# Optimization experiments

Measured on AMD Instinct MI355X. Metric: run time of the kernel, lower is better.

## Reference

```python
import jax
import jax.numpy as jnp
import numpy as np
from jax import lax


def setup_inputs() -> dict:
    key = jax.random.key(0)
    k0, k1 = jax.random.split(key)
    B, C, H, W = 8, 256, 96, 96
    FM0 = jax.random.normal(k0, (B, C, H, W), dtype=jnp.float32)
    FM1 = jax.random.normal(k1, (B, C, H, W), dtype=jnp.float32)
    return {"FM0": FM0, "FM1": FM1, "d_max": 4, "stride": 1}


def pointwise_correlation(FM0, FM1, d_max, stride):
    """out[b,h,w,i,j] = sum_c FM0[b,c,h,w] * FM1[b,c,h+(i-d)*s, w+(j-d)*s],
    with zero padding outside FM1's spatial extent."""
    B, C, H, W = FM0.shape
    D = 2 * d_max + 1
    p = d_max * stride
    FM1p = jnp.pad(FM1, ((0, 0), (0, 0), (p, p), (p, p)))
    offs = jnp.arange(D, dtype=jnp.int32) * stride  # start offsets into padded map
    ys, xs = jnp.meshgrid(offs, offs, indexing="ij")
    offsets = jnp.stack([ys.ravel(), xs.ravel()], axis=-1)  # (D*D, 2)

    def step(carry, off):
        sl = lax.dynamic_slice(FM1p, (0, 0, off[0], off[1]), (B, C, H, W))
        corr = jnp.einsum("bchw,bchw->bhw", FM0, sl)
        return carry, corr

    _, out = lax.scan(step, None, offsets)  # (D*D, B, H, W)
    out = out.reshape(D, D, B, H, W).transpose(2, 3, 4, 0, 1)  # (B, H, W, D, D)
    return out


def reference(FM0, FM1, d_max, stride):
    return pointwise_correlation(FM0, FM1, d_max, stride)
```

## Files before the change

kernel.cpp:

```cpp
#include <hip/hip_runtime.h>

#define HH 96
#define WW 96
#define CC 256
#define PLANE (HH * WW)
#define PITCH 40
#define AROWS 144
#define BROWS 704
#define LDSN ((AROWS + BROWS) * PITCH)
#define NOUT 81
#define NGRP 1696
#define GPT 5

typedef __attribute__((ext_vector_type(4))) float f32x4;
typedef __attribute__((ext_vector_type(2))) unsigned int u32x2;
typedef __attribute__((ext_vector_type(8))) __bf16 bf16x8;

static __device__ __forceinline__ unsigned int pkbf(float x, float y) {
  unsigned int ux = __builtin_bit_cast(unsigned int, x) + 0x8000u;
  unsigned int uy = __builtin_bit_cast(unsigned int, y) + 0x8000u;
  return __builtin_amdgcn_perm(uy, ux, 0x07060302u);
}

#define BAR_LGKM() asm volatile("s_waitcnt lgkmcnt(0)\n\ts_barrier" ::: "memory")

__global__ __launch_bounds__(384, 2) void corr_kernel(
    const float* __restrict__ fm0, const float* __restrict__ fm1,
    float* __restrict__ out) {
  __shared__ __align__(16) unsigned short lds[2 * LDSN];

  const int tid = threadIdx.x;
  const int bid = blockIdx.x;
  const int b = bid & 7;
  const int q = bid >> 3;
  const int s = q & 1;
  const int h0 = 3 * (q >> 1);

  const int lane = tid & 63;
  const int wv = tid >> 6;
  const int mm = lane & 15;
  const int kg = lane >> 4;
  const int a = wv >> 1;
  const int u = wv & 1;

  const size_t boff = (size_t)b * CC * PLANE;

  const float* gptr[GPT];
  int gdst[GPT];
  bool gact[GPT], gok[GPT];
  #pragma unroll
  for (int j = 0; j < GPT; ++j) {
    const int g = tid + 384 * j;
    gact[j] = (g < NGRP);
    if (g < 288) {
      const int ar = g / 96, r = g % 96;
      const int wq = r >> 3, cq = r & 7;
      const int wst = 48 * s + 4 * wq;
      gok[j] = gact[j];
      gdst[j] = (ar * 48 + 4 * wq) * PITCH + 4 * cq;
      gptr[j] = fm0 + boff + (size_t)(4 * cq) * PLANE + (h0 + ar) * WW + wst;
    } else {
      const int gb = g - 288;
      const int i = gb >> 7, r = gb & 127;
      const int wq = r >> 3, cq = r & 7;
      const int hb = h0 - 4 + i;
      const int wst = 48 * s - 8 + 4 * wq;
      const bool ok = (hb >= 0) && (hb < HH) && (wst >= 0) && (wst < WW);
      gok[j] = ok && gact[j];
      gdst[j] = (AROWS + i * 64 + 4 * wq) * PITCH + 4 * cq;
      gptr[j] = fm1 + boff + (size_t)(4 * cq) * PLANE +
                (size_t)(ok ? hb : 0) * WW + (ok ? wst : 0);
    }
  }

  f32x4 pre[GPT][4];
  #pragma unroll
  for (int j = 0; j < GPT; ++j)
    #pragma unroll
    for (int cc = 0; cc < 4; ++cc) pre[j][cc] = f32x4{0.f, 0.f, 0.f, 0.f};

  f32x4 acc[9][3];
  #pragma unroll
  for (int i = 0; i < 9; ++i)
    #pragma unroll
    for (int mt = 0; mt < 3; ++mt) acc[i][mt] = f32x4{0.f, 0.f, 0.f, 0.f};

  const int abase = (a * 48 + mm) * PITCH + kg * 8;
  const int bbase = (AROWS + mm) * PITCH + kg * 8;

  #pragma unroll
  for (int j = 0; j < GPT; ++j)
    if (gok[j]) {
      #pragma unroll
      for (int cc = 0; cc < 4; ++cc)
        pre[j][cc] = *(const f32x4*)(gptr[j] + (size_t)cc * PLANE);
    }
  #pragma unroll
  for (int j = 0; j < GPT; ++j)
    if (gact[j]) {
      #pragma unroll
      for (int dw = 0; dw < 4; ++dw) {
        u32x2 v;
        v.x = pkbf(pre[j][0][dw], pre[j][1][dw]);
        v.y = pkbf(pre[j][2][dw], pre[j][3][dw]);
        *(u32x2*)&lds[gdst[j] + dw * PITCH] = v;
      }
    }
  #pragma unroll
  for (int j = 0; j < GPT; ++j)
    if (gok[j]) {
      #pragma unroll
      for (int cc = 0; cc < 4; ++cc)
        pre[j][cc] = *(const f32x4*)(gptr[j] + (size_t)32 * PLANE +
                                     (size_t)cc * PLANE);
    }
  BAR_LGKM();

  #pragma unroll 1
  for (int ks = 0; ks < 8; ++ks) {
    const int bo = (ks & 1) * LDSN;
    bf16x8 af[3];
    #pragma unroll
    for (int mt = 0; mt < 3; ++mt)
      af[mt] = *(const bf16x8*)&lds[bo + abase + 16 * mt * PITCH];
    #pragma unroll
    for (int i = 0; i < 9; ++i) {
      const int bb = bo + bbase + (a + i) * 64 * PITCH;
      #pragma unroll
      for (int mt = 0; mt < 3; ++mt) {
        bf16x8 bt = *(const bf16x8*)&lds[bb + 16 * (mt + u) * PITCH];
        acc[i][mt] = __builtin_amdgcn_mfma_f32_16x16x32_bf16(af[mt], bt,
                                                             acc[i][mt], 0, 0, 0);
      }
    }
    if (ks < 7) {
      const int bn = ((ks + 1) & 1) * LDSN;
      #pragma unroll
      for (int j = 0; j < GPT; ++j)
        if (gact[j]) {
          #pragma unroll
          for (int dw = 0; dw < 4; ++dw) {
            u32x2 v;
            v.x = pkbf(pre[j][0][dw], pre[j][1][dw]);
            v.y = pkbf(pre[j][2][dw], pre[j][3][dw]);
            *(u32x2*)&lds[bn + gdst[j] + dw * PITCH] = v;
          }
        }
    }
    if (ks < 6) {
      const size_t koff = (size_t)((ks + 2) * 32) * PLANE;
      #pragma unroll
      for (int j = 0; j < GPT; ++j)
        if (gok[j]) {
          #pragma unroll
          for (int cc = 0; cc < 4; ++cc)
            pre[j][cc] = *(const f32x4*)(gptr[j] + koff + (size_t)cc * PLANE);
        }
    }
    BAR_LGKM();
  }

  float* outb = out + ((size_t)b * PLANE + (size_t)(h0 + a) * WW) * NOUT;
  #pragma unroll
  for (int rg = 0; rg < 4; ++rg) {
    const int j = 16 * u + mm - 4 * kg - rg - 4;
    if ((unsigned)j < 9u) {
      #pragma unroll
      for (int i = 0; i < 9; ++i)
        #pragma unroll
        for (int mt = 0; mt < 3; ++mt) {
          const int w = 48 * s + 16 * mt + 4 * kg + rg;
          outb[(size_t)w * NOUT + i * 9 + j] = acc[i][mt][rg];
        }
    }
  }
}

extern "C" void kernel_launch(void* const* d_in, const int* in_sizes, int n_in,
                              void* d_out, int out_size, void* d_ws, size_t ws_size,
                              hipStream_t stream) {
  const float* fm0 = (const float*)d_in[0];
  const float* fm1 = (const float*)d_in[1];
  float* out = (float*)d_out;
  corr_kernel<<<dim3(512), dim3(384), 0, stream>>>(fm0, fm1, out);
}
```

Measured before the change: 212.1 us.

## Retile to 2-row blocks with 16-wide K steps and 16x16x16 bf16 MFMA

Each block now covers 2 output rows with 256 threads, not 3 rows with 384, so the grid grows from 512 to 768 blocks. The LDS pitch is halved and the channel loop runs 16 steps of 16 channels, using the older 16x16x16 bf16 MFMA in place of 16x16x32. Out-of-range halo loads are now issued unconditionally from a valid address and zeroed with a bit mask, which removes per-load branches. The intent is more blocks in flight and less per-block LDS and register pressure. In exchange, the fm1 halo is reloaded more often per output row, there are twice as many barriers and K steps, and the narrower MFMA gives less K per instruction.

```diff
diff --git a/kernel.cpp b/kernel.cpp
--- a/kernel.cpp
+++ b/kernel.cpp
@@ -4,17 +4,19 @@
 #define WW 96
 #define CC 256
 #define PLANE (HH * WW)
-#define PITCH 40
-#define AROWS 144
-#define BROWS 704
-#define LDSN ((AROWS + BROWS) * PITCH)
+#define PITCH 20
+#define AROWS 96
+#define BROWS 640
+#define ROWS (AROWS + BROWS)
+#define LDSN (ROWS * PITCH)
+#define NGRP 736
+#define GPT 3
 #define NOUT 81
-#define NGRP 1696
-#define GPT 5
+#define NKS 16
 
 typedef __attribute__((ext_vector_type(4))) float f32x4;
 typedef __attribute__((ext_vector_type(2))) unsigned int u32x2;
-typedef __attribute__((ext_vector_type(8))) __bf16 bf16x8;
+typedef __attribute__((ext_vector_type(4))) short s16x4;
 
 static __device__ __forceinline__ unsigned int pkbf(float x, float y) {
   unsigned int ux = __builtin_bit_cast(unsigned int, x) + 0x8000u;
@@ -22,9 +24,18 @@
   return __builtin_amdgcn_perm(uy, ux, 0x07060302u);
 }
 
+static __device__ __forceinline__ f32x4 mfma16x16x16bf16(s16x4 a, s16x4 bm, f32x4 c) {
+#if __has_builtin(__builtin_amdgcn_mfma_f32_16x16x16bf16_1k)
+  return __builtin_amdgcn_mfma_f32_16x16x16bf16_1k(a, bm, c, 0, 0, 0);
+#else
+  asm("v_mfma_f32_16x16x16_bf16 %0, %1, %2, %0" : "+v"(c) : "v"(a), "v"(bm));
+  return c;
+#endif
+}
+
 #define BAR_LGKM() asm volatile("s_waitcnt lgkmcnt(0)\n\ts_barrier" ::: "memory")
 
-__global__ __launch_bounds__(384, 2) void corr_kernel(
+__global__ __launch_bounds__(256, 2) void corr_kernel(
     const float* __restrict__ fm0, const float* __restrict__ fm1,
     float* __restrict__ out) {
   __shared__ __align__(16) unsigned short lds[2 * LDSN];
@@ -34,7 +45,7 @@
   const int b = bid & 7;
   const int q = bid >> 3;
   const int s = q & 1;
-  const int h0 = 3 * (q >> 1);
+  const int h0 = 2 * (q >> 1);
 
   const int lane = tid & 63;
   const int wv = tid >> 6;
@@ -47,93 +58,86 @@
 
   const float* gptr[GPT];
   int gdst[GPT];
-  bool gact[GPT], gok[GPT];
+  unsigned int umask[GPT];
+  bool gact[GPT];
   #pragma unroll
   for (int j = 0; j < GPT; ++j) {
-    const int g = tid + 384 * j;
+    const int g = tid + 256 * j;
     gact[j] = (g < NGRP);
-    if (g < 288) {
-      const int ar = g / 96, r = g % 96;
-      const int wq = r >> 3, cq = r & 7;
-      const int wst = 48 * s + 4 * wq;
-      gok[j] = gact[j];
+    bool ok;
+    if (g < AROWS) {
+      const int ar = (g >= 48) ? 1 : 0;
+      const int r = g - 48 * ar;
+      const int wq = r >> 2, cq = r & 3;
+      ok = gact[j];
       gdst[j] = (ar * 48 + 4 * wq) * PITCH + 4 * cq;
-      gptr[j] = fm0 + boff + (size_t)(4 * cq) * PLANE + (h0 + ar) * WW + wst;
+      gptr[j] = fm0 + boff + (size_t)(4 * cq) * PLANE + (h0 + ar) * WW +
+                (48 * s + 4 * wq);
     } else {
-      const int gb = g - 288;
-      const int i = gb >> 7, r = gb & 127;
-      const int wq = r >> 3, cq = r & 7;
-      const int hb = h0 - 4 + i;
+      const int gb = g - AROWS;
+      const int ii = gb >> 6, r = gb & 63;
+      const int wq = r >> 2, cq = r & 3;
+      const int hb = h0 - 4 + ii;
       const int wst = 48 * s - 8 + 4 * wq;
-      const bool ok = (hb >= 0) && (hb < HH) && (wst >= 0) && (wst < WW);
-      gok[j] = ok && gact[j];
-      gdst[j] = (AROWS + i * 64 + 4 * wq) * PITCH + 4 * cq;
+      ok = gact[j] && (hb >= 0) && (hb < HH) && (wst >= 0) && (wst < WW);
+      gdst[j] = (AROWS + ii * 64 + 4 * wq) * PITCH + 4 * cq;
       gptr[j] = fm1 + boff + (size_t)(4 * cq) * PLANE +
                 (size_t)(ok ? hb : 0) * WW + (ok ? wst : 0);
     }
+    umask[j] = ok ? 0xFFFFFFFFu : 0u;
   }
 
   f32x4 pre[GPT][4];
-  #pragma unroll
-  for (int j = 0; j < GPT; ++j)
-    #pragma unroll
-    for (int cc = 0; cc < 4; ++cc) pre[j][cc] = f32x4{0.f, 0.f, 0.f, 0.f};
-
   f32x4 acc[9][3];
   #pragma unroll
   for (int i = 0; i < 9; ++i)
     #pragma unroll
     for (int mt = 0; mt < 3; ++mt) acc[i][mt] = f32x4{0.f, 0.f, 0.f, 0.f};
 
-  const int abase = (a * 48 + mm) * PITCH + kg * 8;
-  const int bbase = (AROWS + mm) * PITCH + kg * 8;
+  const int abase = (a * 48 + mm) * PITCH + kg * 4;
+  const int bbase = (AROWS + mm) * PITCH + kg * 4;
 
   #pragma unroll
   for (int j = 0; j < GPT; ++j)
-    if (gok[j]) {
-      #pragma unroll
-      for (int cc = 0; cc < 4; ++cc)
-        pre[j][cc] = *(const f32x4*)(gptr[j] + (size_t)cc * PLANE);
-    }
+    #pragma unroll
+    for (int cc = 0; cc < 4; ++cc)
+      pre[j][cc] = *(const f32x4*)(gptr[j] + (size_t)cc * PLANE);
   #pragma unroll
   for (int j = 0; j < GPT; ++j)
     if (gact[j]) {
       #pragma unroll
       for (int dw = 0; dw < 4; ++dw) {
         u32x2 v;
-        v.x = pkbf(pre[j][0][dw], pre[j][1][dw]);
-        v.y = pkbf(pre[j][2][dw], pre[j][3][dw]);
+        v.x = pkbf(pre[j][0][dw], pre[j][1][dw]) & umask[j];
+        v.y = pkbf(pre[j][2][dw], pre[j][3][dw]) & umask[j];
         *(u32x2*)&lds[gdst[j] + dw * PITCH] = v;
       }
     }
   #pragma unroll
   for (int j = 0; j < GPT; ++j)
-    if (gok[j]) {
-      #pragma unroll
-      for (int cc = 0; cc < 4; ++cc)
-        pre[j][cc] = *(const f32x4*)(gptr[j] + (size_t)32 * PLANE +
-                                     (size_t)cc * PLANE);
-    }
+    #pragma unroll
+    for (int cc = 0; cc < 4; ++cc)
+      pre[j][cc] = *(const f32x4*)(gptr[j] + (size_t)16 * PLANE +
+                                   (size_t)cc * PLANE);
   BAR_LGKM();
 
   #pragma unroll 1
-  for (int ks = 0; ks < 8; ++ks) {
+  for (int ks = 0; ks < NKS; ++ks) {
     const int bo = (ks & 1) * LDSN;
-    bf16x8 af[3];
+    s16x4 af[3];
     #pragma unroll
     for (int mt = 0; mt < 3; ++mt)
-      af[mt] = *(const bf16x8*)&lds[bo + abase + 16 * mt * PITCH];
+      af[mt] = *(const s16x4*)&lds[bo + abase + 16 * mt * PITCH];
     #pragma unroll
     for (int i = 0; i < 9; ++i) {
       const int bb = bo + bbase + (a + i) * 64 * PITCH;
       #pragma unroll
       for (int mt = 0; mt < 3; ++mt) {
-        bf16x8 bt = *(const bf16x8*)&lds[bb + 16 * (mt + u) * PITCH];
-        acc[i][mt] = __builtin_amdgcn_mfma_f32_16x16x32_bf16(af[mt], bt,
-                                                             acc[i][mt], 0, 0, 0);
+        const s16x4 bt = *(const s16x4*)&lds[bb + 16 * (mt + u) * PITCH];
+        acc[i][mt] = mfma16x16x16bf16(af[mt], bt, acc[i][mt]);
       }
     }
-    if (ks < 7) {
+    if (ks < NKS - 1) {
       const int bn = ((ks + 1) & 1) * LDSN;
       #pragma unroll
       for (int j = 0; j < GPT; ++j)
@@ -141,23 +145,21 @@
           #pragma unroll
           for (int dw = 0; dw < 4; ++dw) {
             u32x2 v;
-            v.x = pkbf(pre[j][0][dw], pre[j][1][dw]);
-            v.y = pkbf(pre[j][2][dw], pre[j][3][dw]);
+            v.x = pkbf(pre[j][0][dw], pre[j][1][dw]) & umask[j];
+            v.y = pkbf(pre[j][2][dw], pre[j][3][dw]) & umask[j];
             *(u32x2*)&lds[bn + gdst[j] + dw * PITCH] = v;
           }
         }
     }
-    if (ks < 6) {
-      const size_t koff = (size_t)((ks + 2) * 32) * PLANE;
+    if (ks < NKS - 2) {
+      const size_t koff = (size_t)((ks + 2) * 16) * PLANE;
       #pragma unroll
       for (int j = 0; j < GPT; ++j)
-        if (gok[j]) {
-          #pragma unroll
-          for (int cc = 0; cc < 4; ++cc)
-            pre[j][cc] = *(const f32x4*)(gptr[j] + koff + (size_t)cc * PLANE);
-        }
+        #pragma unroll
+        for (int cc = 0; cc < 4; ++cc)
+          pre[j][cc] = *(const f32x4*)(gptr[j] + koff + (size_t)cc * PLANE);
     }
-    BAR_LGKM();
+    if (ks < NKS - 1) BAR_LGKM();
   }
 
   float* outb = out + ((size_t)b * PLANE + (size_t)(h0 + a) * WW) * NOUT;
@@ -182,5 +184,5 @@
   const float* fm0 = (const float*)d_in[0];
   const float* fm1 = (const float*)d_in[1];
   float* out = (float*)d_out;
-  corr_kernel<<<dim3(512), dim3(384), 0, stream>>>(fm0, fm1, out);
+  corr_kernel<<<dim3(768), dim3(256), 0, stream>>>(fm0, fm1, out);
 }
```

After: 222.6 us. 1.05x slower.
